# Optimization experiments

Hardware: AMD Instinct MI355X
Metric: run time of the kernel (lower is better)

## Reference

```python
import jax, jax.numpy as jnp
import numpy as np

N_SRC0, N_DST0 = 400000, 100000
N_DST1 = 25000


def _graph_conv(x_src, src, dst, n_dst, W, b):
    # DGL GraphConv, norm='both': h_v = d_in(v)^-1/2 * sum_{u->v} d_out(u)^-1/2 * x_u @ W + b
    ones = jnp.ones(src.shape[0], dtype=x_src.dtype)
    out_deg = jax.ops.segment_sum(ones, src, num_segments=x_src.shape[0])
    in_deg = jax.ops.segment_sum(ones, dst, num_segments=n_dst)
    cs = jnp.where(out_deg > 0, out_deg ** -0.5, 0.0).astype(x_src.dtype)
    cd = jnp.where(in_deg > 0, in_deg ** -0.5, 0.0).astype(x_src.dtype)
    msg = (x_src * cs[:, None])[src]                      # [E, d_in] gather
    agg = jax.ops.segment_sum(msg, dst, num_segments=n_dst)  # [n_dst, d_in] scatter-add
    return (agg * cd[:, None]) @ W + b


def setup_inputs() -> dict:
    key = jax.random.key(0)
    ks = jax.random.split(key, 8)
    E0, E1 = 3200000, 800000
    return {
        "x": jax.random.normal(ks[0], (N_SRC0, 128), dtype=jnp.float32),
        "src0": jax.random.randint(ks[1], (E0,), 0, N_SRC0, dtype=jnp.int32),
        "dst0": jax.random.randint(ks[2], (E0,), 0, N_DST0, dtype=jnp.int32),
        "src1": jax.random.randint(ks[3], (E1,), 0, N_DST0, dtype=jnp.int32),
        "dst1": jax.random.randint(ks[4], (E1,), 0, N_DST1, dtype=jnp.int32),
        "W0": jax.random.normal(ks[5], (128, 256), dtype=jnp.float32) * (128 ** -0.5),
        "b0": jnp.zeros((256,), dtype=jnp.float32),
        "W1": jax.random.normal(ks[6], (256, 64), dtype=jnp.float32) * (256 ** -0.5),
        "b1": jnp.zeros((64,), dtype=jnp.float32),
    }


def reference(x, src0, dst0, src1, dst1, W0, b0, W1, b1):
    h = jax.nn.relu(_graph_conv(x, src0, dst0, N_DST0, W0, b0))   # [N_DST0, 256]
    h = jax.nn.relu(_graph_conv(h, src1, dst1, N_DST1, W1, b1))   # [N_DST1, 64]
    return h
```

## Files before the change

### kernel.cpp

```cpp
#include <hip/hip_runtime.h>
#include <hip/hip_bf16.h>
#include <hip/hip_fp16.h>
#include <stdint.h>

#define N_SRC0 400000
#define N_DST0 100000
#define N_DST1 25000

#define SH_D0 9
#define NK_D0 196
#define SH_S0 9
#define NK_S0 782
#define SH_D1 8
#define NK_D1 98
#define SH_S1 9
#define NK_S1 196
#define NB0 1024
#define NB1 256

#define BH_D0 0
#define BH_S0 (NK_D0 * NB0)
#define BH_D1 (BH_S0 + NK_S0 * NB0)
#define BH_S1 (BH_D1 + NK_D1 * NB1)
#define BH_TOT (BH_S1 + NK_S1 * NB1)

typedef __attribute__((ext_vector_type(8))) short short8;
typedef __attribute__((ext_vector_type(4))) float f32x4;

__device__ __forceinline__ unsigned short f2bf(float f) {
    __hip_bfloat16 h = __float2bfloat16(f);
    union { __hip_bfloat16 h; unsigned short u; } c;
    c.h = h;
    return c.u;
}
__device__ __forceinline__ uint32_t packbf2(float a, float b) {
    return (uint32_t)f2bf(a) | ((uint32_t)f2bf(b) << 16);
}
__device__ __forceinline__ __half2 u2h2(uint32_t u) {
    return __builtin_bit_cast(__half2, u);
}

__device__ __forceinline__ void hist_body(
        const int* __restrict__ src, const int* __restrict__ dst, int n,
        int sshift, int snb, int dshift, int dnb, int NB, int blk,
        int* __restrict__ bhd, int* __restrict__ bhs, int* h) {
    for (int i = threadIdx.x; i < dnb + snb; i += 256) h[i] = 0;
    __syncthreads();
    const int per = (n + NB - 1) / NB;
    const int b = blk * per;
    const int e = min(b + per, n);
    for (int i = b + threadIdx.x; i < e; i += 256) {
        atomicAdd(&h[dst[i] >> dshift], 1);
        atomicAdd(&h[dnb + (src[i] >> sshift)], 1);
    }
    __syncthreads();
    for (int i = threadIdx.x; i < dnb; i += 256) bhd[(size_t)i * NB + blk] = h[i];
    for (int i = threadIdx.x; i < snb; i += 256) bhs[(size_t)i * NB + blk] = h[dnb + i];
}

__global__ __launch_bounds__(256) void hist_fused(
        const int* __restrict__ src0, const int* __restrict__ dst0, int E0,
        const int* __restrict__ src1, const int* __restrict__ dst1, int E1,
        int* __restrict__ bh) {
    extern __shared__ int h[];
    if (blockIdx.x < NB0)
        hist_body(src0, dst0, E0, SH_S0, NK_S0, SH_D0, NK_D0, NB0, blockIdx.x,
                  bh + BH_D0, bh + BH_S0, h);
    else
        hist_body(src1, dst1, E1, SH_S1, NK_S1, SH_D1, NK_D1, NB1, blockIdx.x - NB0,
                  bh + BH_D1, bh + BH_S1, h);
}

#define SCAN_ITEMS 8
#define SCAN_TILE 2048

__global__ __launch_bounds__(256) void scan1_kernel(
        const int* __restrict__ in, int* __restrict__ out,
        int* __restrict__ sums, int n) {
    __shared__ int lds[256];
    const int tid = threadIdx.x;
    const int base = blockIdx.x * SCAN_TILE + tid * SCAN_ITEMS;
    int v[SCAN_ITEMS];
    int run = 0;
    #pragma unroll
    for (int i = 0; i < SCAN_ITEMS; ++i) {
        int t = (base + i < n) ? in[base + i] : 0;
        v[i] = run;
        run += t;
    }
    lds[tid] = run;
    __syncthreads();
    int incl = run;
    for (int off = 1; off < 256; off <<= 1) {
        int u = (tid >= off) ? lds[tid - off] : 0;
        __syncthreads();
        incl += u;
        lds[tid] = incl;
        __syncthreads();
    }
    if (tid == 255) sums[blockIdx.x] = incl;
    int excl = incl - run;
    #pragma unroll
    for (int i = 0; i < SCAN_ITEMS; ++i)
        if (base + i < n) out[base + i] = excl + v[i];
}

__global__ __launch_bounds__(256) void scan2_kernel(int* __restrict__ sums, int nb) {
    __shared__ int lds[256];
    const int tid = threadIdx.x;
    const int base = tid * 4;
    int v[4];
    int run = 0;
    #pragma unroll
    for (int i = 0; i < 4; ++i) {
        int t = (base + i < nb) ? sums[base + i] : 0;
        v[i] = run;
        run += t;
    }
    lds[tid] = run;
    __syncthreads();
    int incl = run;
    for (int off = 1; off < 256; off <<= 1) {
        int u = (tid >= off) ? lds[tid - off] : 0;
        __syncthreads();
        incl += u;
        lds[tid] = incl;
        __syncthreads();
    }
    int excl = incl - run;
    #pragma unroll
    for (int i = 0; i < 4; ++i)
        if (base + i < nb) sums[base + i] = excl + v[i];
}

__global__ void scan3_kernel(int* __restrict__ out, const int* __restrict__ sums, int n) {
    int i = blockIdx.x * blockDim.x + threadIdx.x;
    if (i < n) out[i] += sums[i / SCAN_TILE];
}

__device__ __forceinline__ void scat_body(
        const int* __restrict__ src, const int* __restrict__ dst, int n,
        int sshift, int snb, int dshift, int dnb, int NB, int blk, int ksh,
        const int* __restrict__ bhd, const int* __restrict__ bhs,
        uint32_t* __restrict__ stg, int* cur) {
    for (int i = threadIdx.x; i < dnb; i += 256) cur[i] = bhd[(size_t)i * NB + blk];
    for (int i = threadIdx.x; i < snb; i += 256) cur[dnb + i] = bhs[(size_t)i * NB + blk];
    __syncthreads();
    const int per = (n + NB - 1) / NB;
    const int b = blk * per;
    const int e = min(b + per, n);
    const int dmask = (1 << dshift) - 1;
    for (int i = b + threadIdx.x; i < e; i += 256) {
        int s = src[i], d = dst[i];
        int pd = atomicAdd(&cur[d >> dshift], 1);
        stg[pd] = ((uint32_t)(d & dmask) << ksh) | (uint32_t)s;
        int ps = atomicAdd(&cur[dnb + (s >> sshift)], 1);
        stg[ps] = (uint32_t)s;
    }
}

__global__ __launch_bounds__(256) void scat_fused(
        const int* __restrict__ src0, const int* __restrict__ dst0, int E0,
        const int* __restrict__ src1, const int* __restrict__ dst1, int E1,
        const int* __restrict__ bh, uint32_t* __restrict__ stg) {
    extern __shared__ int cur[];
    if (blockIdx.x < NB0)
        scat_body(src0, dst0, E0, SH_S0, NK_S0, SH_D0, NK_D0, NB0, blockIdx.x, 19,
                  bh + BH_D0, bh + BH_S0, stg, cur);
    else
        scat_body(src1, dst1, E1, SH_S1, NK_S1, SH_D1, NK_D1, NB1, blockIdx.x - NB0, 17,
                  bh + BH_D1, bh + BH_S1, stg, cur);
}

__device__ __forceinline__ void fine_csr_body(
        const uint32_t* __restrict__ stg, const int* __restrict__ bht,
        int NB, int shift, int ksh, int nbins, int total, int rel, int nbkt, int k,
        int* __restrict__ off, int* __restrict__ esrc, int* fine, int* part) {
    const int fb = 1 << shift;
    const int base = bht[(size_t)k * NB];
    const int end = (k + 1 < nbkt) ? bht[(size_t)(k + 1) * NB] : total;
    const int gb = k << shift;
    const int t = threadIdx.x;
    const uint32_t mask = (1u << ksh) - 1;
    for (int i = t; i < fb; i += 256) fine[i] = 0;
    __syncthreads();
    for (int i = base + t; i < end; i += 256)
        atomicAdd(&fine[stg[i] >> ksh], 1);
    __syncthreads();
    int a0 = (2 * t < fb) ? fine[2 * t] : 0;
    int a1 = (2 * t + 1 < fb) ? fine[2 * t + 1] : 0;
    part[t] = a0 + a1;
    __syncthreads();
    int incl = part[t];
    for (int o = 1; o < 256; o <<= 1) {
        int u = (t >= o) ? part[t - o] : 0;
        __syncthreads();
        incl += u;
        part[t] = incl;
        __syncthreads();
    }
    int excl = incl - (a0 + a1);
    if (2 * t < fb) fine[2 * t] = excl;
    if (2 * t + 1 < fb) fine[2 * t + 1] = excl + a0;
    __syncthreads();
    const int rb = base - rel;
    for (int i = t; i < fb; i += 256) {
        int g = gb + i;
        if (g < nbins) off[g] = rb + fine[i];
    }
    if (k == nbkt - 1 && t == 0) off[nbins] = total - rel;
    __syncthreads();
    for (int i = base + t; i < end; i += 256) {
        uint32_t v = stg[i];
        int p = atomicAdd(&fine[v >> ksh], 1);
        esrc[rb + p] = (int)(v & mask);
    }
}

__device__ __forceinline__ void fine_deg_body(
        const uint32_t* __restrict__ stg, const int* __restrict__ bht,
        int NB, int shift, int nbins, int total, int nbkt, int k,
        float* __restrict__ csf, int* fine) {
    const int fb = 1 << shift;
    const int base = bht[(size_t)k * NB];
    const int end = (k + 1 < nbkt) ? bht[(size_t)(k + 1) * NB] : total;
    const int gb = k << shift;
    for (int i = threadIdx.x; i < fb; i += 256) fine[i] = 0;
    __syncthreads();
    for (int i = base + threadIdx.x; i < end; i += 256)
        atomicAdd(&fine[(int)stg[i] - gb], 1);
    __syncthreads();
    for (int i = threadIdx.x; i < fb; i += 256) {
        int g = gb + i;
        if (g < nbins) {
            int c = fine[i];
            csf[g] = c > 0 ? rsqrtf((float)c) : 0.f;
        }
    }
}

__global__ __launch_bounds__(256) void fine_fused(
        const uint32_t* __restrict__ stg, const int* __restrict__ bh,
        int E0, int E1,
        int* __restrict__ off0, int* __restrict__ esrc0,
        int* __restrict__ off1, int* __restrict__ esrc1,
        float* __restrict__ cs0, float* __restrict__ cs1,
        const float* __restrict__ W0, const float* __restrict__ W1,
        unsigned short* __restrict__ W0p, unsigned short* __restrict__ W1p) {
    __shared__ int fine[512];
    __shared__ int part[256];
    int kb = blockIdx.x;
    if (kb < NK_D0) {
        fine_csr_body(stg, bh + BH_D0, NB0, SH_D0, 19, N_DST0, E0, 0, NK_D0, kb,
                      off0, esrc0, fine, part);
        return;
    }
    kb -= NK_D0;
    if (kb < NK_S0) {
        fine_deg_body(stg, bh + BH_S0, NB0, SH_S0, N_SRC0, 2 * E0, NK_S0, kb,
                      cs0, fine);
        return;
    }
    kb -= NK_S0;
    if (kb < NK_D1) {
        fine_csr_body(stg, bh + BH_D1, NB1, SH_D1, 17, N_DST1, 2 * E0 + E1, 2 * E0, NK_D1, kb,
                      off1, esrc1, fine, part);
        return;
    }
    kb -= NK_D1;
    if (kb < NK_S1) {
        fine_deg_body(stg, bh + BH_S1, NB1, SH_S1, N_DST0, 2 * E0 + 2 * E1, NK_S1, kb,
                      cs1, fine);
        return;
    }
    kb -= NK_S1;
    if (kb < 128) {
        int id = kb * 256 + threadIdx.x;
        int kk = id & 31, n2 = (id >> 5) & 255, kt = id >> 13;
        W0p[id] = f2bf(W0[(kt * 32 + kk) * 256 + n2]);
    } else {
        int id = (kb - 128) * 256 + threadIdx.x;
        int kk = id & 31, n2 = (id >> 5) & 63, kt = id >> 11;
        W1p[id] = f2bf(W1[(kt * 32 + kk) * 64 + n2]);
    }
}

__global__ __launch_bounds__(256) void prescale_kernel(
        const float4* __restrict__ x4, const float* __restrict__ cs,
        uint2* __restrict__ xs) {
    int id = blockIdx.x * 256 + threadIdx.x;
    int row = id >> 5;
    float c = cs[row];
    float4 v = x4[id];
    uint2 o;
    o.x = __builtin_bit_cast(uint32_t, __floats2half2_rn(v.x * c, v.y * c));
    o.y = __builtin_bit_cast(uint32_t, __floats2half2_rn(v.z * c, v.w * c));
    xs[id] = o;
}

__global__ __launch_bounds__(256) void agg0_kernel(
        const uint32_t* __restrict__ xs, const int* __restrict__ esrc,
        const int* __restrict__ off, uint32_t* __restrict__ aggb) {
    const int row = blockIdx.x * 4 + (threadIdx.x >> 6);
    const uint32_t t = threadIdx.x & 63;
    const int b = off[row], e = off[row + 1];
    const __half2 z = __builtin_bit_cast(__half2, 0u);
    __half2 a[16];
    #pragma unroll
    for (int k = 0; k < 16; ++k) a[k] = z;
    int i = b;
    for (; i + 15 < e; i += 16) {
        uint32_t idx[16];
        #pragma unroll
        for (int k = 0; k < 16; ++k)
            idx[k] = ((uint32_t)esrc[i + k] << 6) + t;
        #pragma unroll
        for (int k = 0; k < 16; ++k)
            a[k] = __hadd2(a[k], u2h2(xs[idx[k]]));
    }
    for (; i + 3 < e; i += 4) {
        #pragma unroll
        for (int k = 0; k < 4; ++k)
            a[k] = __hadd2(a[k], u2h2(xs[((uint32_t)esrc[i + k] << 6) + t]));
    }
    for (; i < e; ++i)
        a[0] = __hadd2(a[0], u2h2(xs[((uint32_t)esrc[i] << 6) + t]));
    #pragma unroll
    for (int k = 0; k < 8; ++k) a[k] = __hadd2(a[k], a[k + 8]);
    #pragma unroll
    for (int k = 0; k < 4; ++k) a[k] = __hadd2(a[k], a[k + 4]);
    __half2 s = __hadd2(__hadd2(a[0], a[1]), __hadd2(a[2], a[3]));
    float cd = (e > b) ? rsqrtf((float)(e - b)) : 0.f;
    aggb[(size_t)row * 64 + t] = packbf2(__low2float(s) * cd, __high2float(s) * cd);
}

__global__ __launch_bounds__(256) void gemm01_mfma(
        const short* __restrict__ A,
        const short* __restrict__ B0p,
        const float* __restrict__ bias0,
        const short* __restrict__ B1p,
        const float* __restrict__ cs1,
        __half* __restrict__ Y) {
    __shared__ short hs[32][264];
    const int w = threadIdx.x >> 6;
    const int l = threadIdx.x & 63;
    const int rbase = blockIdx.x * 32;
    const int lr = l & 15;
    const int lk = (l >> 4) * 8;
    const int orow0 = (l >> 4) * 4;

    {
        const int cbase = w * 64;
        f32x4 acc[2][4] = {};
        #pragma unroll
        for (int kt = 0; kt < 4; ++kt) {
            short8 a[2], b[4];
            #pragma unroll
            for (int rt = 0; rt < 2; ++rt)
                a[rt] = *(const short8*)(A + (size_t)(rbase + rt * 16 + lr) * 128 + kt * 32 + lk);
            #pragma unroll
            for (int ct = 0; ct < 4; ++ct)
                b[ct] = *(const short8*)(B0p + (size_t)(kt * 256 + cbase + ct * 16 + lr) * 32 + lk);
            #pragma unroll
            for (int rt = 0; rt < 2; ++rt)
                #pragma unroll
                for (int ct = 0; ct < 4; ++ct)
                    acc[rt][ct] = __builtin_amdgcn_mfma_f32_16x16x32_bf16(a[rt], b[ct], acc[rt][ct], 0, 0, 0);
        }
        #pragma unroll
        for (int rt = 0; rt < 2; ++rt) {
            #pragma unroll
            for (int ct = 0; ct < 4; ++ct) {
                int col = cbase + ct * 16 + lr;
                float bv = bias0[col];
                #pragma unroll
                for (int j = 0; j < 4; ++j)
                    hs[rt * 16 + orow0 + j][col] = (short)f2bf(fmaxf(acc[rt][ct][j] + bv, 0.f));
            }
        }
    }
    __syncthreads();

    {
        f32x4 acc2[2] = {};
        #pragma unroll
        for (int kt = 0; kt < 8; ++kt) {
            short8 b1 = *(const short8*)(B1p + (size_t)(kt * 64 + w * 16 + lr) * 32 + lk);
            #pragma unroll
            for (int rt = 0; rt < 2; ++rt) {
                short8 av = *(const short8*)(&hs[rt * 16 + lr][kt * 32 + lk]);
                acc2[rt] = __builtin_amdgcn_mfma_f32_16x16x32_bf16(av, b1, acc2[rt], 0, 0, 0);
            }
        }
        #pragma unroll
        for (int rt = 0; rt < 2; ++rt) {
            #pragma unroll
            for (int j = 0; j < 4; ++j) {
                int row = rbase + rt * 16 + orow0 + j;
                float c = cs1[row];
                Y[(size_t)row * 64 + w * 16 + lr] = __float2half(acc2[rt][j] * c);
            }
        }
    }
}

__global__ __launch_bounds__(256) void agg1_kernel(
        const uint2* __restrict__ y2, const int* __restrict__ esrc,
        const int* __restrict__ off, const float* __restrict__ bias,
        float* __restrict__ out, int nrows) {
    int row = blockIdx.x * 16 + (threadIdx.x >> 4);
    int t = threadIdx.x & 15;
    if (row >= nrows) return;
    int b = off[row], e = off[row + 1];
    const __half2 z = __builtin_bit_cast(__half2, 0u);
    __half2 aA0 = z, aA1 = z, aB0 = z, aB1 = z;
    int i = b;
    for (; i + 8 <= e; i += 8) {
        #pragma unroll
        for (int k = 0; k < 8; k += 2) {
            int s0 = esrc[i + k], s1 = esrc[i + k + 1];
            uint2 v0 = y2[(size_t)s0 * 16 + t];
            uint2 v1 = y2[(size_t)s1 * 16 + t];
            aA0 = __hadd2(aA0, u2h2(v0.x));
            aA1 = __hadd2(aA1, u2h2(v0.y));
            aB0 = __hadd2(aB0, u2h2(v1.x));
            aB1 = __hadd2(aB1, u2h2(v1.y));
        }
    }
    for (; i < e; ++i) {
        uint2 v = y2[(size_t)esrc[i] * 16 + t];
        aA0 = __hadd2(aA0, u2h2(v.x));
        aA1 = __hadd2(aA1, u2h2(v.y));
    }
    float cd = (e > b) ? rsqrtf((float)(e - b)) : 0.f;
    __half2 s0 = __hadd2(aA0, aB0), s1 = __hadd2(aA1, aB1);
    float4 bv = *(const float4*)(bias + t * 4);
    float4 o;
    o.x = fmaxf(__low2float(s0) * cd + bv.x, 0.f);
    o.y = fmaxf(__high2float(s0) * cd + bv.y, 0.f);
    o.z = fmaxf(__low2float(s1) * cd + bv.z, 0.f);
    o.w = fmaxf(__high2float(s1) * cd + bv.w, 0.f);
    *(float4*)(out + (size_t)row * 64 + t * 4) = o;
}

extern "C" void kernel_launch(void* const* d_in, const int* in_sizes, int n_in,
                              void* d_out, int out_size, void* d_ws, size_t ws_size,
                              hipStream_t stream) {
    const float* x    = (const float*)d_in[0];
    const int*   src0 = (const int*)d_in[1];
    const int*   dst0 = (const int*)d_in[2];
    const int*   src1 = (const int*)d_in[3];
    const int*   dst1 = (const int*)d_in[4];
    const float* W0   = (const float*)d_in[5];
    const float* b0   = (const float*)d_in[6];
    const float* W1   = (const float*)d_in[7];
    const float* b1   = (const float*)d_in[8];
    float* out = (float*)d_out;

    const int E0 = in_sizes[1];
    const int E1 = in_sizes[3];

    char* p = (char*)d_ws;
    auto alloc = [&](size_t bytes) {
        char* r = p;
        p += (bytes + 511) & ~(size_t)511;
        return r;
    };
    int*   bh    = (int*)alloc((size_t)BH_TOT * 4);
    int*   sums  = (int*)alloc(1024 * 4);
    int*   off0  = (int*)alloc((size_t)(N_DST0 + 1) * 4);
    int*   off1  = (int*)alloc((size_t)(N_DST1 + 1) * 4);
    float* cs0   = (float*)alloc((size_t)N_SRC0 * 4);
    float* cs1   = (float*)alloc((size_t)N_DST0 * 4);
    int*   esrc0 = (int*)alloc((size_t)E0 * 4);
    int*   esrc1 = (int*)alloc((size_t)E1 * 4);
    unsigned short* W0p = (unsigned short*)alloc((size_t)32768 * 2);
    unsigned short* W1p = (unsigned short*)alloc((size_t)16384 * 2);
    size_t bigA = (size_t)N_SRC0 * 128 * 2;
    size_t bigB = (size_t)N_DST0 * 128 * 2;
    size_t bigStg = (size_t)(2 * E0 + 2 * E1) * 4;
    size_t bigSz = bigA + bigB;
    if (bigStg > bigSz) bigSz = bigStg;
    char* big = alloc(bigSz);

    uint32_t* stg  = (uint32_t*)big;
    uint2*    xs   = (uint2*)big;
    __half*   y1b  = (__half*)big;
    uint32_t* aggb = (uint32_t*)(big + bigA);

    hist_fused<<<NB0 + NB1, 256, (NK_D0 + NK_S0) * 4, stream>>>(
        src0, dst0, E0, src1, dst1, E1, bh);
    const int nsb = (BH_TOT + SCAN_TILE - 1) / SCAN_TILE;
    scan1_kernel<<<nsb, 256, 0, stream>>>(bh, bh, sums, BH_TOT);
    scan2_kernel<<<1, 256, 0, stream>>>(sums, nsb);
    scan3_kernel<<<(BH_TOT + 255) / 256, 256, 0, stream>>>(bh, sums, BH_TOT);
    scat_fused<<<NB0 + NB1, 256, (NK_D0 + NK_S0) * 4, stream>>>(
        src0, dst0, E0, src1, dst1, E1, bh, stg);
    fine_fused<<<NK_D0 + NK_S0 + NK_D1 + NK_S1 + 192, 256, 0, stream>>>(
        stg, bh, E0, E1, off0, esrc0, off1, esrc1, cs0, cs1, W0, W1, W0p, W1p);

    prescale_kernel<<<N_SRC0 * 32 / 256, 256, 0, stream>>>((const float4*)x, cs0, xs);

    agg0_kernel<<<N_DST0 / 4, 256, 0, stream>>>(
        (const uint32_t*)xs, esrc0, off0, aggb);

    gemm01_mfma<<<N_DST0 / 32, 256, 0, stream>>>(
        (const short*)aggb, (const short*)W0p, b0, (const short*)W1p, cs1, y1b);

    agg1_kernel<<<(N_DST1 + 15) / 16, 256, 0, stream>>>(
        (const uint2*)y1b, esrc1, off1, b1, out, N_DST1);
}
```

Before: 388.9 us.

## Fold scan block sums into consumers, split staging arrays, halve histogram blocks

Drops the third scan pass and adds the block-level prefix sums directly where bucket offsets are read in the scatter and fine kernels. The staging buffer is split into per-graph destination (32-bit) and source (16-bit local index) arrays, so source-degree staging uses half the bytes. The block counts for the histogram and scatter halve, which shrinks the histogram table and scan work but gives each block more edges to process serially. The fold assumes a scan tile of 2048, so correctness depends on that constant matching SCAN_TILE.

New measurement: 381.4 us. Within noise of the previous version (-1.9%).

```diff
diff --git a/kernel.cpp b/kernel.cpp
--- a/kernel.cpp
+++ b/kernel.cpp
@@ -15,8 +15,8 @@
 #define NK_D1 98
 #define SH_S1 9
 #define NK_S1 196
-#define NB0 1024
-#define NB1 256
+#define NB0 512
+#define NB1 128
 
 #define BH_D0 0
 #define BH_S0 (NK_D0 * NB0)
@@ -133,52 +133,66 @@
         if (base + i < nb) sums[base + i] = excl + v[i];
 }
 
-__global__ void scan3_kernel(int* __restrict__ out, const int* __restrict__ sums, int n) {
-    int i = blockIdx.x * blockDim.x + threadIdx.x;
-    if (i < n) out[i] += sums[i / SCAN_TILE];
-}
-
 __device__ __forceinline__ void scat_body(
         const int* __restrict__ src, const int* __restrict__ dst, int n,
         int sshift, int snb, int dshift, int dnb, int NB, int blk, int ksh,
         const int* __restrict__ bhd, const int* __restrict__ bhs,
-        uint32_t* __restrict__ stg, int* cur) {
-    for (int i = threadIdx.x; i < dnb; i += 256) cur[i] = bhd[(size_t)i * NB + blk];
-    for (int i = threadIdx.x; i < snb; i += 256) cur[dnb + i] = bhs[(size_t)i * NB + blk];
+        const int* __restrict__ sums, int goffd, int goffs, int Td, int Ts,
+        uint32_t* __restrict__ stg_d, unsigned short* __restrict__ stg_s, int* cur) {
+    for (int i = threadIdx.x; i < dnb; i += 256) {
+        int gi = goffd + i * NB + blk;
+        cur[i] = bhd[(size_t)i * NB + blk] + sums[gi >> 11] - Td;
+    }
+    for (int i = threadIdx.x; i < snb; i += 256) {
+        int gi = goffs + i * NB + blk;
+        cur[dnb + i] = bhs[(size_t)i * NB + blk] + sums[gi >> 11] - Ts;
+    }
     __syncthreads();
     const int per = (n + NB - 1) / NB;
     const int b = blk * per;
     const int e = min(b + per, n);
     const int dmask = (1 << dshift) - 1;
+    const int smask = (1 << sshift) - 1;
     for (int i = b + threadIdx.x; i < e; i += 256) {
         int s = src[i], d = dst[i];
         int pd = atomicAdd(&cur[d >> dshift], 1);
-        stg[pd] = ((uint32_t)(d & dmask) << ksh) | (uint32_t)s;
+        stg_d[pd] = ((uint32_t)(d & dmask) << ksh) | (uint32_t)s;
         int ps = atomicAdd(&cur[dnb + (s >> sshift)], 1);
-        stg[ps] = (uint32_t)s;
+        stg_s[ps] = (unsigned short)(s & smask);
     }
 }
 
 __global__ __launch_bounds__(256) void scat_fused(
         const int* __restrict__ src0, const int* __restrict__ dst0, int E0,
         const int* __restrict__ src1, const int* __restrict__ dst1, int E1,
-        const int* __restrict__ bh, uint32_t* __restrict__ stg) {
+        const int* __restrict__ bh, const int* __restrict__ sums,
+        uint32_t* __restrict__ stgd0, unsigned short* __restrict__ stgs0,
+        uint32_t* __restrict__ stgd1, unsigned short* __restrict__ stgs1) {
     extern __shared__ int cur[];
     if (blockIdx.x < NB0)
         scat_body(src0, dst0, E0, SH_S0, NK_S0, SH_D0, NK_D0, NB0, blockIdx.x, 19,
-                  bh + BH_D0, bh + BH_S0, stg, cur);
+                  bh + BH_D0, bh + BH_S0, sums, BH_D0, BH_S0, 0, E0,
+                  stgd0, stgs0, cur);
     else
         scat_body(src1, dst1, E1, SH_S1, NK_S1, SH_D1, NK_D1, NB1, blockIdx.x - NB0, 17,
-                  bh + BH_D1, bh + BH_S1, stg, cur);
+                  bh + BH_D1, bh + BH_S1, sums, BH_D1, BH_S1, 2 * E0, 2 * E0 + E1,
+                  stgd1, stgs1, cur);
+}
+
+__device__ __forceinline__ int fold_base(const int* bht, const int* sums,
+                                         int goff, int NB, int T, int k) {
+    int gi = goff + k * NB;
+    return bht[(size_t)k * NB] + sums[gi >> 11] - T;
 }
 
 __device__ __forceinline__ void fine_csr_body(
         const uint32_t* __restrict__ stg, const int* __restrict__ bht,
-        int NB, int shift, int ksh, int nbins, int total, int rel, int nbkt, int k,
+        const int* __restrict__ sums, int goff, int T,
+        int NB, int shift, int ksh, int nbins, int total, int nbkt, int k,
         int* __restrict__ off, int* __restrict__ esrc, int* fine, int* part) {
     const int fb = 1 << shift;
-    const int base = bht[(size_t)k * NB];
-    const int end = (k + 1 < nbkt) ? bht[(size_t)(k + 1) * NB] : total;
+    const int base = fold_base(bht, sums, goff, NB, T, k);
+    const int end = (k + 1 < nbkt) ? fold_base(bht, sums, goff, NB, T, k + 1) : total;
     const int gb = k << shift;
     const int t = threadIdx.x;
     const uint32_t mask = (1u << ksh) - 1;
@@ -203,32 +217,32 @@
     if (2 * t < fb) fine[2 * t] = excl;
     if (2 * t + 1 < fb) fine[2 * t + 1] = excl + a0;
     __syncthreads();
-    const int rb = base - rel;
     for (int i = t; i < fb; i += 256) {
         int g = gb + i;
-        if (g < nbins) off[g] = rb + fine[i];
-    }
-    if (k == nbkt - 1 && t == 0) off[nbins] = total - rel;
+        if (g < nbins) off[g] = base + fine[i];
+    }
+    if (k == nbkt - 1 && t == 0) off[nbins] = total;
     __syncthreads();
     for (int i = base + t; i < end; i += 256) {
         uint32_t v = stg[i];
         int p = atomicAdd(&fine[v >> ksh], 1);
-        esrc[rb + p] = (int)(v & mask);
+        esrc[base + p] = (int)(v & mask);
     }
 }
 
 __device__ __forceinline__ void fine_deg_body(
-        const uint32_t* __restrict__ stg, const int* __restrict__ bht,
+        const unsigned short* __restrict__ stg, const int* __restrict__ bht,
+        const int* __restrict__ sums, int goff, int T,
         int NB, int shift, int nbins, int total, int nbkt, int k,
         float* __restrict__ csf, int* fine) {
     const int fb = 1 << shift;
-    const int base = bht[(size_t)k * NB];
-    const int end = (k + 1 < nbkt) ? bht[(size_t)(k + 1) * NB] : total;
+    const int base = fold_base(bht, sums, goff, NB, T, k);
+    const int end = (k + 1 < nbkt) ? fold_base(bht, sums, goff, NB, T, k + 1) : total;
     const int gb = k << shift;
     for (int i = threadIdx.x; i < fb; i += 256) fine[i] = 0;
     __syncthreads();
     for (int i = base + threadIdx.x; i < end; i += 256)
-        atomicAdd(&fine[(int)stg[i] - gb], 1);
+        atomicAdd(&fine[stg[i]], 1);
     __syncthreads();
     for (int i = threadIdx.x; i < fb; i += 256) {
         int g = gb + i;
@@ -240,7 +254,9 @@
 }
 
 __global__ __launch_bounds__(256) void fine_fused(
-        const uint32_t* __restrict__ stg, const int* __restrict__ bh,
+        const uint32_t* __restrict__ stgd0, const unsigned short* __restrict__ stgs0,
+        const uint32_t* __restrict__ stgd1, const unsigned short* __restrict__ stgs1,
+        const int* __restrict__ bh, const int* __restrict__ sums,
         int E0, int E1,
         int* __restrict__ off0, int* __restrict__ esrc0,
         int* __restrict__ off1, int* __restrict__ esrc1,
@@ -251,26 +267,26 @@
     __shared__ int part[256];
     int kb = blockIdx.x;
     if (kb < NK_D0) {
-        fine_csr_body(stg, bh + BH_D0, NB0, SH_D0, 19, N_DST0, E0, 0, NK_D0, kb,
-                      off0, esrc0, fine, part);
+        fine_csr_body(stgd0, bh + BH_D0, sums, BH_D0, 0,
+                      NB0, SH_D0, 19, N_DST0, E0, NK_D0, kb, off0, esrc0, fine, part);
         return;
     }
     kb -= NK_D0;
     if (kb < NK_S0) {
-        fine_deg_body(stg, bh + BH_S0, NB0, SH_S0, N_SRC0, 2 * E0, NK_S0, kb,
-                      cs0, fine);
+        fine_deg_body(stgs0, bh + BH_S0, sums, BH_S0, E0,
+                      NB0, SH_S0, N_SRC0, E0, NK_S0, kb, cs0, fine);
         return;
     }
     kb -= NK_S0;
     if (kb < NK_D1) {
-        fine_csr_body(stg, bh + BH_D1, NB1, SH_D1, 17, N_DST1, 2 * E0 + E1, 2 * E0, NK_D1, kb,
-                      off1, esrc1, fine, part);
+        fine_csr_body(stgd1, bh + BH_D1, sums, BH_D1, 2 * E0,
+                      NB1, SH_D1, 17, N_DST1, E1, NK_D1, kb, off1, esrc1, fine, part);
         return;
     }
     kb -= NK_D1;
     if (kb < NK_S1) {
-        fine_deg_body(stg, bh + BH_S1, NB1, SH_S1, N_DST0, 2 * E0 + 2 * E1, NK_S1, kb,
-                      cs1, fine);
+        fine_deg_body(stgs1, bh + BH_S1, sums, BH_S1, 2 * E0 + E1,
+                      NB1, SH_S1, N_DST0, E1, NK_S1, kb, cs1, fine);
         return;
     }
     kb -= NK_S1;
@@ -478,12 +494,22 @@
     unsigned short* W1p = (unsigned short*)alloc((size_t)16384 * 2);
     size_t bigA = (size_t)N_SRC0 * 128 * 2;
     size_t bigB = (size_t)N_DST0 * 128 * 2;
-    size_t bigStg = (size_t)(2 * E0 + 2 * E1) * 4;
+    size_t bigStg = (size_t)(E0 * 6 + E1 * 6 + 1024);
     size_t bigSz = bigA + bigB;
     if (bigStg > bigSz) bigSz = bigStg;
     char* big = alloc(bigSz);
 
-    uint32_t* stg  = (uint32_t*)big;
+    char* q = big;
+    auto carve = [&](size_t bytes) {
+        char* r = q;
+        q += (bytes + 511) & ~(size_t)511;
+        return r;
+    };
+    uint32_t*       stgd0 = (uint32_t*)carve((size_t)E0 * 4);
+    unsigned short* stgs0 = (unsigned short*)carve((size_t)E0 * 2);
+    uint32_t*       stgd1 = (uint32_t*)carve((size_t)E1 * 4);
+    unsigned short* stgs1 = (unsigned short*)carve((size_t)E1 * 2);
+
     uint2*    xs   = (uint2*)big;
     __half*   y1b  = (__half*)big;
     uint32_t* aggb = (uint32_t*)(big + bigA);
@@ -493,11 +519,11 @@
     const int nsb = (BH_TOT + SCAN_TILE - 1) / SCAN_TILE;
     scan1_kernel<<<nsb, 256, 0, stream>>>(bh, bh, sums, BH_TOT);
     scan2_kernel<<<1, 256, 0, stream>>>(sums, nsb);
-    scan3_kernel<<<(BH_TOT + 255) / 256, 256, 0, stream>>>(bh, sums, BH_TOT);
     scat_fused<<<NB0 + NB1, 256, (NK_D0 + NK_S0) * 4, stream>>>(
-        src0, dst0, E0, src1, dst1, E1, bh, stg);
+        src0, dst0, E0, src1, dst1, E1, bh, sums, stgd0, stgs0, stgd1, stgs1);
     fine_fused<<<NK_D0 + NK_S0 + NK_D1 + NK_S1 + 192, 256, 0, stream>>>(
-        stg, bh, E0, E1, off0, esrc0, off1, esrc1, cs0, cs1, W0, W1, W0p, W1p);
+        stgd0, stgs0, stgd1, stgs1, bh, sums, E0, E1,
+        off0, esrc0, off1, esrc1, cs0, cs1, W0, W1, W0p, W1p);
 
     prescale_kernel<<<N_SRC0 * 32 / 256, 256, 0, stream>>>((const float4*)x, cs0, xs);
 
```
